# Kernel optimization log

Hardware: AMD Instinct MI355X
Metric: run time of the kernel (lower is better)

The kernel has to match this reference:

```python
import jax, jax.numpy as jnp
import numpy as np

GRID_MIN, GRID_MAX, NUM_GRIDS = -2.0, 2.0, 8
DENOM = (GRID_MAX - GRID_MIN) / (NUM_GRIDS - 1)
DIM, NUM_HEADS = 768, 12
B, N = 8, 1024


def _layer_norm(x, w, b, eps=1e-5):
    mu = jnp.mean(x, axis=-1, keepdims=True)
    var = jnp.mean((x - mu) ** 2, axis=-1, keepdims=True)
    return (x - mu) * jax.lax.rsqrt(var + eps) * w + b


def _fastkan(x, ln_w, ln_b, spline_w, base_w, base_b):
    # x: [..., C]; spline_w: [C*G, O]; base_w: [C, O]
    grid = jnp.linspace(GRID_MIN, GRID_MAX, NUM_GRIDS, dtype=x.dtype)
    h = _layer_norm(x, ln_w, ln_b)
    # RBF basis expansion: [..., C, G]
    basis = jnp.exp(-(((h[..., None] - grid) / DENOM) ** 2))
    basis = basis.reshape(*basis.shape[:-2], -1)  # [..., C*G]
    ret = basis @ spline_w
    ret = ret + jax.nn.silu(x) @ base_w + base_b
    return ret


def setup_inputs() -> dict:
    key = jax.random.key(0)
    ks = jax.random.split(key, 6)
    C = DIM
    return {
        "x": jax.random.normal(ks[0], (B, N, C), jnp.float32),
        "qkv_ln_w": jnp.ones((C,), jnp.float32),
        "qkv_ln_b": jnp.zeros((C,), jnp.float32),
        "qkv_spline_w": jax.random.normal(ks[1], (C * NUM_GRIDS, 3 * C), jnp.float32) * 0.1,
        "qkv_base_w": jax.random.normal(ks[2], (C, 3 * C), jnp.float32) * (1.0 / np.sqrt(C)),
        "qkv_base_b": jnp.zeros((3 * C,), jnp.float32),
        "proj_ln_w": jnp.ones((C,), jnp.float32),
        "proj_ln_b": jnp.zeros((C,), jnp.float32),
        "proj_spline_w": jax.random.normal(ks[3], (C * NUM_GRIDS, C), jnp.float32) * 0.1,
        "proj_base_w": jax.random.normal(ks[4], (C, C), jnp.float32) * (1.0 / np.sqrt(C)),
        "proj_base_b": jnp.zeros((C,), jnp.float32),
    }


def reference(x, qkv_ln_w, qkv_ln_b, qkv_spline_w, qkv_base_w, qkv_base_b,
              proj_ln_w, proj_ln_b, proj_spline_w, proj_base_w, proj_base_b):
    b, n, c = x.shape
    h = NUM_HEADS
    d = c // h
    scale = d ** -0.5
    qkv = _fastkan(x, qkv_ln_w, qkv_ln_b, qkv_spline_w, qkv_base_w, qkv_base_b)
    qkv = qkv.reshape(b, n, 3, h, d).transpose(2, 0, 3, 1, 4)  # [3,B,H,N,D]
    q, k, v = qkv[0], qkv[1], qkv[2]
    attn = jnp.einsum("bhnd,bhmd->bhnm", q, k) * scale
    attn = jax.nn.softmax(attn, axis=-1)
    out = jnp.einsum("bhnm,bhmd->bhnd", attn, v)
    out = out.transpose(0, 2, 1, 3).reshape(b, n, c)
    out = _fastkan(out, proj_ln_w, proj_ln_b, proj_spline_w, proj_base_w, proj_base_b)
    return out
```

## Files before the change

kernel.cpp:

```cpp
#include <hip/hip_runtime.h>
#include <cstdint>
#include <cstddef>

typedef _Float16 h8 __attribute__((ext_vector_type(8)));
typedef float f4 __attribute__((ext_vector_type(4)));
typedef float f16f __attribute__((ext_vector_type(16)));

#define DEV static __device__ __forceinline__

DEV void gld16(const void* g, void* l) {
  __builtin_amdgcn_global_load_lds(
      (const __attribute__((address_space(1))) void*)g,
      (__attribute__((address_space(3))) void*)l, 16, 0, 0);
}

__global__ __launch_bounds__(256)
void kan_prep(const float* __restrict__ X, const float* __restrict__ lnw,
              const float* __restrict__ lnb, _Float16* __restrict__ Acat) {
  const int row = blockIdx.x;
  const int tid = threadIdx.x;
  const float* xr = X + (size_t)row * 768;
  float xv[3];
  xv[0] = xr[tid]; xv[1] = xr[tid + 256]; xv[2] = xr[tid + 512];
  float s = xv[0] + xv[1] + xv[2];
  float q = xv[0] * xv[0] + xv[1] * xv[1] + xv[2] * xv[2];
#pragma unroll
  for (int off = 32; off; off >>= 1) {
    s += __shfl_xor(s, off);
    q += __shfl_xor(q, off);
  }
  __shared__ float rs_[4], rq_[4];
  const int wave = tid >> 6;
  if ((tid & 63) == 0) { rs_[wave] = s; rq_[wave] = q; }
  __syncthreads();
  s = rs_[0] + rs_[1] + rs_[2] + rs_[3];
  q = rq_[0] + rq_[1] + rq_[2] + rq_[3];
  const float mu = s * (1.0f / 768.0f);
  const float var = q * (1.0f / 768.0f) - mu * mu;
  const float rsig = rsqrtf(var + 1e-5f);
  _Float16* out = Acat + (size_t)row * 6912;
#pragma unroll
  for (int i = 0; i < 3; ++i) {
    const int c = tid + i * 256;
    const float x = xv[i];
    const float h = (x - mu) * rsig * lnw[c] + lnb[c];
    union { h8 v; _Float16 u[8]; } bs;
#pragma unroll
    for (int g = 0; g < 8; ++g) {
      const float gv = -2.0f + (4.0f / 7.0f) * (float)g;
      const float t = (h - gv) * 1.75f;
      bs.u[g] = (_Float16)__expf(-t * t);
    }
    *(h8*)(out + c * 8) = bs.v;
    out[6144 + c] = (_Float16)(x / (1.0f + __expf(-x)));
  }
}

__global__ __launch_bounds__(256)
void wt_cast(const float* __restrict__ W, _Float16* __restrict__ Bp,
             int N, int koff, int nkt) {
  __shared__ float t[32][33];
  const int k0 = blockIdx.x * 32, n0 = blockIdx.y * 32;
  const int tx = threadIdx.x & 31, ty = threadIdx.x >> 5;
#pragma unroll
  for (int i = 0; i < 4; ++i)
    t[ty + i * 8][tx] = W[(size_t)(k0 + ty + i * 8) * N + n0 + tx];
  __syncthreads();
  const int f = threadIdx.x;
  if (f < 128) {
    const int nn = f & 31, cc = f >> 5;
    union { h8 v; _Float16 u[8]; } bs;
#pragma unroll
    for (int j = 0; j < 8; ++j) bs.u[j] = (_Float16)t[cc * 8 + j][nn];
    const int kg = koff + k0 + cc * 8;
    const int nt = (n0 + nn) >> 5;
    const size_t addr = ((size_t)nt * nkt + (kg >> 6)) * 2048 +
                        (size_t)((((kg >> 4) & 3) * 64 + nn + 32 * ((kg >> 3) & 1))) * 8;
    *(h8*)(Bp + addr) = bs.v;
  }
}

__global__ __launch_bounds__(256)
void v_transpose(const _Float16* __restrict__ qkv, _Float16* __restrict__ Vt) {
  const int bh = blockIdx.z, hh = bh % 12, b = bh / 12;
  const int kvb = blockIdx.x * 32, db = blockIdx.y * 32;
  __shared__ _Float16 t[32][33];
  const int tx = threadIdx.x & 31, ty = threadIdx.x >> 5;
#pragma unroll
  for (int i = 0; i < 4; ++i) {
    const int kv = kvb + ty + i * 8;
    t[ty + i * 8][tx] = qkv[(size_t)(b * 1024 + kv) * 2304 + 1536 + hh * 64 + db + tx];
  }
  __syncthreads();
#pragma unroll
  for (int i = 0; i < 4; ++i) {
    const int d = db + ty + i * 8;
    Vt[(size_t)(bh * 64 + d) * 1024 + kvb + tx] = t[tx][ty + i * 8];
  }
}

#define LOAD_B(dst)                                       \
  {                                                       \
    _Pragma("unroll") for (int ni = 0; ni < 2; ++ni) {    \
      _Pragma("unroll") for (int ks = 0; ks < 4; ++ks)    \
        dst[ni][ks] = *(const h8*)(bpp[ni] + ks * 512);   \
      bpp[ni] += 2048;                                    \
    }                                                     \
  }
#define LOAD_A(buf)                                       \
  {                                                       \
    _Pragma("unroll") for (int i = 0; i < 4; ++i) {       \
      gld16(ap[i], (buf) + alOff[i]);                     \
      ap[i] += 64;                                        \
    }                                                     \
  }
#define MFMA_STEP(buf, br)                                \
  {                                                       \
    const h8* A8 = (const h8*)(buf);                      \
    _Pragma("unroll") for (int ks = 0; ks < 4; ++ks) {    \
      const int o = (ks * 2 + half) ^ swz;                \
      h8 af0 = A8[(wm + l31) * 8 + o];                    \
      h8 af1 = A8[(wm + 32 + l31) * 8 + o];               \
      acc[0][0] = __builtin_amdgcn_mfma_f32_32x32x16_f16(af0, br[0][ks], acc[0][0], 0, 0, 0); \
      acc[0][1] = __builtin_amdgcn_mfma_f32_32x32x16_f16(af0, br[1][ks], acc[0][1], 0, 0, 0); \
      acc[1][0] = __builtin_amdgcn_mfma_f32_32x32x16_f16(af1, br[0][ks], acc[1][0], 0, 0, 0); \
      acc[1][1] = __builtin_amdgcn_mfma_f32_32x32x16_f16(af1, br[1][ks], acc[1][1], 0, 0, 0); \
    }                                                     \
  }

template <bool F16OUT>
__global__ __launch_bounds__(256, 2)
void gemm_bt(const _Float16* __restrict__ A, const _Float16* __restrict__ Bp,
             const float* __restrict__ bias, void* __restrict__ Cout,
             int N, int ldK, int kLen, size_t sliceStride) {
  __shared__ __align__(16) _Float16 As[2 * 128 * 64];
  _Float16* As0 = As;
  _Float16* As1 = As + 128 * 64;
  const int tid = threadIdx.x;
  const int lane = tid & 63, wave = tid >> 6;
  const int gx = gridDim.x;
  const int lin = blockIdx.y * gx + blockIdx.x;
  const int xcd = lin & 7, pos = lin >> 3;
  const int bandH = gridDim.y >> 3;
  const int bm = (xcd * bandH + pos / gx) * 128;
  const int bn = (pos % gx) * 128;
  const int slice = blockIdx.z;
  const int kOff = slice * kLen;
  const int rsub = lane >> 3;
  const int l7 = lane & 7;
  const int l31 = lane & 31, half = lane >> 5;
  const int wm = (wave >> 1) * 64, wn = (wave & 1) * 64;
  const _Float16* ap[4];
  int alOff[4];
#pragma unroll
  for (int i = 0; i < 4; ++i) {
    const int ch = wave * 4 + i;
    const int ksw = (l7 ^ rsub ^ ((ch & 3) << 1)) * 8;
    ap[i] = A + (size_t)(bm + ch * 8 + rsub) * ldK + kOff + ksw;
    alOff[i] = ch * 512;
  }
  const size_t nktTot = (size_t)(ldK >> 6);
  const int kt0 = kOff >> 6;
  const _Float16* bpp[2];
#pragma unroll
  for (int ni = 0; ni < 2; ++ni)
    bpp[ni] = Bp + ((size_t)((bn >> 5) + (wn >> 5) + ni) * nktTot + kt0) * 2048 + lane * 8;

  f16f acc[2][2] = {};
  const int swz = l7 ^ ((rsub & 3) << 1);
  const int nkt = kLen >> 6;
  h8 bregA[2][4], bregB[2][4];
  LOAD_B(bregA);
  LOAD_A(As0);
  for (int kt = 0; kt < nkt; kt += 2) {
    __syncthreads();
    if (kt + 1 < nkt) { LOAD_B(bregB); LOAD_A(As1); }
    MFMA_STEP(As0, bregA);
    __syncthreads();
    if (kt + 2 < nkt) { LOAD_B(bregA); LOAD_A(As0); }
    MFMA_STEP(As1, bregB);
  }
#pragma unroll
  for (int ni = 0; ni < 2; ++ni) {
    const int col = bn + wn + ni * 32 + l31;
    const float bv = F16OUT ? bias[col] : 0.0f;
#pragma unroll
    for (int mi = 0; mi < 2; ++mi) {
      const int rb = bm + wm + mi * 32 + 4 * half;
#pragma unroll
      for (int reg = 0; reg < 16; ++reg) {
        const int r = rb + (reg & 3) + 8 * (reg >> 2);
        const float v = acc[mi][ni][reg] + bv;
        if (F16OUT)
          ((_Float16*)Cout)[(size_t)r * N + col] = (_Float16)v;
        else
          ((float*)Cout + slice * sliceStride)[(size_t)r * N + col] = v;
      }
    }
  }
}

__global__ __launch_bounds__(256)
void ksum2(const float* __restrict__ P, const float* __restrict__ bias,
           float* __restrict__ out) {
  const size_t off = ((size_t)blockIdx.x * 256 + threadIdx.x) * 4;
  const int col = (int)(off % 768);
  f4 a = *(const f4*)(P + off);
  f4 b = *(const f4*)(P + (size_t)8192 * 768 + off);
  f4 c = *(const f4*)(bias + col);
  *(f4*)(out + off) = a + b + c;
}

__global__ __launch_bounds__(256)
void attn(const _Float16* __restrict__ qkv, const _Float16* __restrict__ Vt,
          float* __restrict__ ctx) {
  __shared__ __align__(16) _Float16 Qs[128 * 64];
  __shared__ __align__(16) _Float16 Ks[64 * 64];
  __shared__ __align__(16) _Float16 Vs[64 * 64];
  __shared__ __align__(16) _Float16 Ps[4 * 32 * 72];
  const int tid = threadIdx.x;
  const int lane = tid & 63, wave = tid >> 6;
  const int bh = blockIdx.y, hh = bh % 12, b = bh / 12;
  const int qt = blockIdx.x;
  const int rsub = lane >> 3;
  const int ksw = ((lane & 7) ^ rsub) * 8;
#pragma unroll
  for (int i = 0; i < 4; ++i) {
    const int ch = wave * 4 + i;
    const int row = ch * 8 + rsub;
    gld16(qkv + (size_t)(b * 1024 + qt * 128 + row) * 2304 + hh * 64 + ksw, Qs + ch * 512);
  }
  const int l16 = lane & 15, quad = lane >> 4, r7 = l16 & 7;
  f4 acc_o[2][4] = {};
  float m_old[2][4], l_sum[2][4];
#pragma unroll
  for (int mi = 0; mi < 2; ++mi)
#pragma unroll
    for (int j = 0; j < 4; ++j) { m_old[mi][j] = -1e30f; l_sum[mi][j] = 0.0f; }

  _Float16* Pw = Ps + wave * (32 * 72);

  for (int kv0 = 0; kv0 < 1024; kv0 += 64) {
#pragma unroll
    for (int i = 0; i < 2; ++i) {
      const int ch = wave * 2 + i;
      const int row = ch * 8 + rsub;
      gld16(qkv + (size_t)(b * 1024 + kv0 + row) * 2304 + 768 + hh * 64 + ksw, Ks + ch * 512);
      gld16(Vt + (size_t)(bh * 64 + row) * 1024 + kv0 + ksw, Vs + ch * 512);
    }
    __syncthreads();
    const h8* Q8 = (const h8*)Qs;
    const h8* K8 = (const h8*)Ks;
    const h8* V8 = (const h8*)Vs;
    f4 s[2][4] = {};
#pragma unroll
    for (int ks = 0; ks < 2; ++ks) {
      const int kq = (ks * 4 + quad) ^ r7;
      h8 qf[2], kf[4];
#pragma unroll
      for (int mi = 0; mi < 2; ++mi) qf[mi] = Q8[(wave * 32 + mi * 16 + l16) * 8 + kq];
#pragma unroll
      for (int ni = 0; ni < 4; ++ni) kf[ni] = K8[(ni * 16 + l16) * 8 + kq];
#pragma unroll
      for (int mi = 0; mi < 2; ++mi)
#pragma unroll
        for (int ni = 0; ni < 4; ++ni)
          s[mi][ni] = __builtin_amdgcn_mfma_f32_16x16x32_f16(qf[mi], kf[ni], s[mi][ni], 0, 0, 0);
    }
#pragma unroll
    for (int mi = 0; mi < 2; ++mi)
#pragma unroll
      for (int ni = 0; ni < 4; ++ni) s[mi][ni] *= 0.125f;
#pragma unroll
    for (int mi = 0; mi < 2; ++mi) {
#pragma unroll
      for (int j = 0; j < 4; ++j) {
        float vm = fmaxf(fmaxf(s[mi][0][j], s[mi][1][j]), fmaxf(s[mi][2][j], s[mi][3][j]));
#pragma unroll
        for (int off = 1; off < 16; off <<= 1) vm = fmaxf(vm, __shfl_xor(vm, off));
        const float mn = fmaxf(m_old[mi][j], vm);
        const float alpha = __expf(m_old[mi][j] - mn);
        float rs = 0.0f;
#pragma unroll
        for (int ni = 0; ni < 4; ++ni) {
          const float p = __expf(s[mi][ni][j] - mn);
          s[mi][ni][j] = p;
          rs += p;
        }
#pragma unroll
        for (int off = 1; off < 16; off <<= 1) rs += __shfl_xor(rs, off);
        l_sum[mi][j] = l_sum[mi][j] * alpha + rs;
        m_old[mi][j] = mn;
#pragma unroll
        for (int ni = 0; ni < 4; ++ni) acc_o[mi][ni][j] *= alpha;
      }
    }
#pragma unroll
    for (int mi = 0; mi < 2; ++mi)
#pragma unroll
      for (int ni = 0; ni < 4; ++ni)
#pragma unroll
        for (int j = 0; j < 4; ++j)
          Pw[(mi * 16 + quad * 4 + j) * 72 + ni * 16 + l16] = (_Float16)s[mi][ni][j];
#pragma unroll
    for (int ks = 0; ks < 2; ++ks) {
      const int kq = ks * 4 + quad;
      h8 pf[2], vf[4];
#pragma unroll
      for (int mi = 0; mi < 2; ++mi) pf[mi] = *(const h8*)(Pw + (mi * 16 + l16) * 72 + kq * 8);
#pragma unroll
      for (int ni = 0; ni < 4; ++ni) vf[ni] = V8[(ni * 16 + l16) * 8 + (kq ^ r7)];
#pragma unroll
      for (int mi = 0; mi < 2; ++mi)
#pragma unroll
        for (int ni = 0; ni < 4; ++ni)
          acc_o[mi][ni] = __builtin_amdgcn_mfma_f32_16x16x32_f16(pf[mi], vf[ni], acc_o[mi][ni], 0, 0, 0);
    }
    __syncthreads();
  }
#pragma unroll
  for (int mi = 0; mi < 2; ++mi) {
#pragma unroll
    for (int j = 0; j < 4; ++j) {
      const float inv = 1.0f / l_sum[mi][j];
      const int tok = b * 1024 + qt * 128 + wave * 32 + mi * 16 + quad * 4 + j;
      float* cr = ctx + (size_t)tok * 768 + hh * 64;
#pragma unroll
      for (int ni = 0; ni < 4; ++ni) cr[ni * 16 + l16] = acc_o[mi][ni][j] * inv;
    }
  }
}

extern "C" void kernel_launch(void* const* d_in, const int* in_sizes, int n_in,
                              void* d_out, int out_size, void* d_ws, size_t ws_size,
                              hipStream_t stream) {
  (void)in_sizes; (void)n_in; (void)out_size; (void)ws_size;
  const float* x    = (const float*)d_in[0];
  const float* qlnw = (const float*)d_in[1];
  const float* qlnb = (const float*)d_in[2];
  const float* qsw  = (const float*)d_in[3];
  const float* qbw  = (const float*)d_in[4];
  const float* qbb  = (const float*)d_in[5];
  const float* plnw = (const float*)d_in[6];
  const float* plnb = (const float*)d_in[7];
  const float* psw  = (const float*)d_in[8];
  const float* pbw  = (const float*)d_in[9];
  const float* pbb  = (const float*)d_in[10];
  float* out = (float*)d_out;

  _Float16* WtQ  = (_Float16*)d_ws;
  _Float16* WtP  = WtQ + (size_t)2304 * 6912;
  _Float16* Acat = WtP + (size_t)768 * 6912;
  _Float16* QKV  = Acat + (size_t)8192 * 6912;
  _Float16* Vt   = QKV + (size_t)8192 * 2304;
  float* CTX = (float*)(Vt + (size_t)96 * 64 * 1024);
  float* Pp = (float*)QKV;

  dim3 blk(256);
  wt_cast<<<dim3(192, 72), blk, 0, stream>>>(qsw, WtQ, 2304, 0, 108);
  wt_cast<<<dim3(24, 72),  blk, 0, stream>>>(qbw, WtQ, 2304, 6144, 108);
  wt_cast<<<dim3(192, 24), blk, 0, stream>>>(psw, WtP, 768, 0, 108);
  wt_cast<<<dim3(24, 24),  blk, 0, stream>>>(pbw, WtP, 768, 6144, 108);
  kan_prep<<<8192, blk, 0, stream>>>(x, qlnw, qlnb, Acat);
  gemm_bt<true><<<dim3(2304 / 128, 8192 / 128, 1), blk, 0, stream>>>(
      Acat, WtQ, qbb, QKV, 2304, 6912, 6912, 0);
  v_transpose<<<dim3(32, 2, 96), blk, 0, stream>>>(QKV, Vt);
  attn<<<dim3(8, 96), blk, 0, stream>>>(QKV, Vt, CTX);
  kan_prep<<<8192, blk, 0, stream>>>(CTX, plnw, plnb, Acat);
  gemm_bt<false><<<dim3(768 / 128, 8192 / 128, 2), blk, 0, stream>>>(
      Acat, WtP, nullptr, Pp, 768, 6912, 3456, (size_t)8192 * 768);
  ksum2<<<8192 * 768 / 4 / 256, blk, 0, stream>>>(Pp, pbb, out);
}
```

Before: 712.1 us.

## Use 8-wave 256x128 tile GEMM with priority-boosted MFMA for QKV projection

Adds a new gemm8 kernel with 512 threads per block and a 256x128 output tile for the QKV KAN GEMM. B fragments go straight into registers through double-buffered register sets, and A is double-buffered in LDS. Synchronisation uses explicit waitcnt/barrier and sched_barrier, and s_setprio is raised around the MFMA sections. The larger tile increases reuse of the B fragments and halves the grid along M. In exchange it uses more LDS and registers per block, which may lower occupancy, and the hand-tuned wait counts carry a correctness risk.

```diff
diff --git a/kernel.cpp b/kernel.cpp
--- a/kernel.cpp
+++ b/kernel.cpp
@@ -127,6 +127,91 @@
       acc[1][1] = __builtin_amdgcn_mfma_f32_32x32x16_f16(af1, br[1][ks], acc[1][1], 0, 0, 0); \
     }                                                     \
   }
+#define SB() __builtin_amdgcn_sched_barrier(0)
+#define WAITBAR()                                                        \
+  {                                                                      \
+    asm volatile("s_waitcnt vmcnt(8) lgkmcnt(0)" ::: "memory");          \
+    __builtin_amdgcn_s_barrier();                                        \
+    asm volatile("" ::: "memory");                                       \
+  }
+#define COMPUTE(buf, br)                                  \
+  {                                                       \
+    __builtin_amdgcn_s_setprio(1);                        \
+    MFMA_STEP(buf, br);                                   \
+    __builtin_amdgcn_s_setprio(0);                        \
+  }
+
+__global__ __launch_bounds__(512, 2)
+void gemm8(const _Float16* __restrict__ A, const _Float16* __restrict__ Bp,
+           const float* __restrict__ bias, _Float16* __restrict__ Cout,
+           int N, int ldK) {
+  __shared__ __align__(16) _Float16 As[2 * 256 * 64];
+  _Float16* As0 = As;
+  _Float16* As1 = As + 256 * 64;
+  const int tid = threadIdx.x;
+  const int lane = tid & 63, wave = tid >> 6;
+  const int gx = gridDim.x;
+  const int lin = blockIdx.y * gx + blockIdx.x;
+  const int xcd = lin & 7, pos = lin >> 3;
+  const int bandH = gridDim.y >> 3;
+  const int bm = (xcd * bandH + pos / gx) * 256;
+  const int bn = (pos % gx) * 128;
+  const int rsub = lane >> 3;
+  const int l7 = lane & 7;
+  const int l31 = lane & 31, half = lane >> 5;
+  const int wm = (wave >> 1) * 64, wn = (wave & 1) * 64;
+  const _Float16* ap[4];
+  int alOff[4];
+#pragma unroll
+  for (int i = 0; i < 4; ++i) {
+    const int ch = wave * 4 + i;
+    const int ksw = (l7 ^ rsub ^ ((ch & 3) << 1)) * 8;
+    ap[i] = A + (size_t)(bm + ch * 8 + rsub) * ldK + ksw;
+    alOff[i] = ch * 512;
+  }
+  const size_t nktTot = (size_t)(ldK >> 6);
+  const _Float16* bpp[2];
+#pragma unroll
+  for (int ni = 0; ni < 2; ++ni)
+    bpp[ni] = Bp + (size_t)((bn >> 5) + (wn >> 5) + ni) * nktTot * 2048 + lane * 8;
+
+  f16f acc[2][2] = {};
+  const int swz = l7 ^ ((rsub & 3) << 1);
+  const int nkt = ldK >> 6;
+  h8 bregA[2][4], bregB[2][4];
+  LOAD_A(As0); SB();
+  LOAD_B(bregA); SB();
+  WAITBAR();
+  for (int kt = 0; kt < nkt - 2; kt += 2) {
+    LOAD_A(As1); SB();
+    LOAD_B(bregB); SB();
+    COMPUTE(As0, bregA);
+    WAITBAR();
+    LOAD_A(As0); SB();
+    LOAD_B(bregA); SB();
+    COMPUTE(As1, bregB);
+    WAITBAR();
+  }
+  LOAD_A(As1); SB();
+  LOAD_B(bregB); SB();
+  COMPUTE(As0, bregA);
+  WAITBAR();
+  COMPUTE(As1, bregB);
+#pragma unroll
+  for (int ni = 0; ni < 2; ++ni) {
+    const int col = bn + wn + ni * 32 + l31;
+    const float bv = bias[col];
+#pragma unroll
+    for (int mi = 0; mi < 2; ++mi) {
+      const int rb = bm + wm + mi * 32 + 4 * half;
+#pragma unroll
+      for (int reg = 0; reg < 16; ++reg) {
+        const int r = rb + (reg & 3) + 8 * (reg >> 2);
+        Cout[(size_t)r * N + col] = (_Float16)(acc[mi][ni][reg] + bv);
+      }
+    }
+  }
+}
 
 template <bool F16OUT>
 __global__ __launch_bounds__(256, 2)
@@ -362,8 +447,8 @@
   wt_cast<<<dim3(192, 24), blk, 0, stream>>>(psw, WtP, 768, 0, 108);
   wt_cast<<<dim3(24, 24),  blk, 0, stream>>>(pbw, WtP, 768, 6144, 108);
   kan_prep<<<8192, blk, 0, stream>>>(x, qlnw, qlnb, Acat);
-  gemm_bt<true><<<dim3(2304 / 128, 8192 / 128, 1), blk, 0, stream>>>(
-      Acat, WtQ, qbb, QKV, 2304, 6912, 6912, 0);
+  gemm8<<<dim3(2304 / 128, 8192 / 256), dim3(512), 0, stream>>>(
+      Acat, WtQ, qbb, QKV, 2304, 6912);
   v_transpose<<<dim3(32, 2, 96), blk, 0, stream>>>(QKV, Vt);
   attn<<<dim3(8, 96), blk, 0, stream>>>(QKV, Vt, CTX);
   kan_prep<<<8192, blk, 0, stream>>>(CTX, plnw, plnb, Acat);
```

New measurement: 789.6 us. 10.9% more time.

## Triple-buffer A tiles in GEMM with explicit vmcnt waits and sched barriers

Applied to the files above, without the earlier changes.

Replaces the double-buffered LDS pipeline in the GEMM kernel with a three-stage ring buffer. A tiles are prefetched two steps ahead, and each step waits on a partial vmcnt count instead of a full __syncthreads, with sched_barrier pinning the instruction order. The aim is to keep more global loads in flight and hide their latency behind the MFMAs. It uses 50% more LDS per block, which can lower occupancy, and the hard-coded epilogue assumes nkt is large enough and follows a specific stage pattern.

```diff
diff --git a/kernel.cpp b/kernel.cpp
--- a/kernel.cpp
+++ b/kernel.cpp
@@ -127,15 +127,21 @@
       acc[1][1] = __builtin_amdgcn_mfma_f32_32x32x16_f16(af1, br[1][ks], acc[1][1], 0, 0, 0); \
     }                                                     \
   }
+#define SB() __builtin_amdgcn_sched_barrier(0)
+#define WB(n)                                                          \
+  {                                                                    \
+    asm volatile("s_waitcnt vmcnt(" #n ") lgkmcnt(0)" ::: "memory");   \
+    __builtin_amdgcn_s_barrier();                                      \
+    SB();                                                              \
+  }
 
 template <bool F16OUT>
 __global__ __launch_bounds__(256, 2)
 void gemm_bt(const _Float16* __restrict__ A, const _Float16* __restrict__ Bp,
              const float* __restrict__ bias, void* __restrict__ Cout,
              int N, int ldK, int kLen, size_t sliceStride) {
-  __shared__ __align__(16) _Float16 As[2 * 128 * 64];
-  _Float16* As0 = As;
-  _Float16* As1 = As + 128 * 64;
+  __shared__ __align__(16) _Float16 As[3 * 128 * 64];
+  _Float16* const bufs[3] = {As, As + 8192, As + 16384};
   const int tid = threadIdx.x;
   const int lane = tid & 63, wave = tid >> 6;
   const int gx = gridDim.x;
@@ -170,16 +176,23 @@
   const int swz = l7 ^ ((rsub & 3) << 1);
   const int nkt = kLen >> 6;
   h8 bregA[2][4], bregB[2][4];
-  LOAD_B(bregA);
-  LOAD_A(As0);
-  for (int kt = 0; kt < nkt; kt += 2) {
-    __syncthreads();
-    if (kt + 1 < nkt) { LOAD_B(bregB); LOAD_A(As1); }
-    MFMA_STEP(As0, bregA);
-    __syncthreads();
-    if (kt + 2 < nkt) { LOAD_B(bregA); LOAD_A(As0); }
-    MFMA_STEP(As1, bregB);
-  }
+  LOAD_A(bufs[0]); SB();
+  LOAD_A(bufs[1]); SB();
+  LOAD_B(bregA); SB();
+  for (int kt = 0; kt < nkt - 6; kt += 6) {
+    WB(12); LOAD_B(bregB); SB(); LOAD_A(bufs[2]); SB(); MFMA_STEP(bufs[0], bregA);
+    WB(12); LOAD_B(bregA); SB(); LOAD_A(bufs[0]); SB(); MFMA_STEP(bufs[1], bregB);
+    WB(12); LOAD_B(bregB); SB(); LOAD_A(bufs[1]); SB(); MFMA_STEP(bufs[2], bregA);
+    WB(12); LOAD_B(bregA); SB(); LOAD_A(bufs[2]); SB(); MFMA_STEP(bufs[0], bregB);
+    WB(12); LOAD_B(bregB); SB(); LOAD_A(bufs[0]); SB(); MFMA_STEP(bufs[1], bregA);
+    WB(12); LOAD_B(bregA); SB(); LOAD_A(bufs[1]); SB(); MFMA_STEP(bufs[2], bregB);
+  }
+  WB(12); LOAD_B(bregB); SB(); LOAD_A(bufs[2]); SB(); MFMA_STEP(bufs[0], bregA);
+  WB(12); LOAD_B(bregA); SB(); LOAD_A(bufs[0]); SB(); MFMA_STEP(bufs[1], bregB);
+  WB(12); LOAD_B(bregB); SB(); LOAD_A(bufs[1]); SB(); MFMA_STEP(bufs[2], bregA);
+  WB(12); LOAD_B(bregA); SB(); LOAD_A(bufs[2]); SB(); MFMA_STEP(bufs[0], bregB);
+  WB(12); LOAD_B(bregB); SB();                        MFMA_STEP(bufs[1], bregA);
+  WB(8);                                              MFMA_STEP(bufs[2], bregB);
 #pragma unroll
   for (int ni = 0; ni < 2; ++ni) {
     const int col = bn + wn + ni * 32 + l31;
```

Result: slower. 741.4 us (+4.1%).

## Triple-buffer GEMM A tiles and double-buffer attention K/V with Q in registers

Applied to the files above, without the earlier changes.

The GEMM moves from a two-stage to a three-stage LDS ring for A tiles, using explicit vmcnt-based waits plus barriers so that two tile loads stay in flight during MFMA work. The attention kernel keeps Q fragments in registers instead of LDS, double-buffers K/V so the next tile is prefetched while the current one is computed, folds the 1/8 scale into the exp argument, and raises wave priority around MFMA sections. The aim is to hide global-load latency and cut barrier stalls. The cost is more LDS in the GEMM, which may lower occupancy. The hand-written waitcnt counts are fragile: they assume a fixed number of outstanding loads per stage.

```diff
diff --git a/kernel.cpp b/kernel.cpp
--- a/kernel.cpp
+++ b/kernel.cpp
@@ -127,15 +127,21 @@
       acc[1][1] = __builtin_amdgcn_mfma_f32_32x32x16_f16(af1, br[1][ks], acc[1][1], 0, 0, 0); \
     }                                                     \
   }
+#define WB(n)                                                          \
+  {                                                                    \
+    asm volatile("s_waitcnt vmcnt(" #n ") lgkmcnt(0)" ::: "memory");   \
+    __builtin_amdgcn_s_barrier();                                      \
+  }
 
 template <bool F16OUT>
 __global__ __launch_bounds__(256, 2)
 void gemm_bt(const _Float16* __restrict__ A, const _Float16* __restrict__ Bp,
              const float* __restrict__ bias, void* __restrict__ Cout,
              int N, int ldK, int kLen, size_t sliceStride) {
-  __shared__ __align__(16) _Float16 As[2 * 128 * 64];
-  _Float16* As0 = As;
-  _Float16* As1 = As + 128 * 64;
+  __shared__ __align__(16) _Float16 As[3 * 128 * 64];
+  _Float16* const b0 = As;
+  _Float16* const b1 = As + 8192;
+  _Float16* const b2 = As + 16384;
   const int tid = threadIdx.x;
   const int lane = tid & 63, wave = tid >> 6;
   const int gx = gridDim.x;
@@ -170,16 +176,23 @@
   const int swz = l7 ^ ((rsub & 3) << 1);
   const int nkt = kLen >> 6;
   h8 bregA[2][4], bregB[2][4];
+  LOAD_A(b0);
+  LOAD_A(b1);
   LOAD_B(bregA);
-  LOAD_A(As0);
-  for (int kt = 0; kt < nkt; kt += 2) {
-    __syncthreads();
-    if (kt + 1 < nkt) { LOAD_B(bregB); LOAD_A(As1); }
-    MFMA_STEP(As0, bregA);
-    __syncthreads();
-    if (kt + 2 < nkt) { LOAD_B(bregA); LOAD_A(As0); }
-    MFMA_STEP(As1, bregB);
-  }
+  for (int kt = 0; kt < nkt - 6; kt += 6) {
+    WB(12); LOAD_B(bregB); LOAD_A(b2); MFMA_STEP(b0, bregA);
+    WB(12); LOAD_B(bregA); LOAD_A(b0); MFMA_STEP(b1, bregB);
+    WB(12); LOAD_B(bregB); LOAD_A(b1); MFMA_STEP(b2, bregA);
+    WB(12); LOAD_B(bregA); LOAD_A(b2); MFMA_STEP(b0, bregB);
+    WB(12); LOAD_B(bregB); LOAD_A(b0); MFMA_STEP(b1, bregA);
+    WB(12); LOAD_B(bregA); LOAD_A(b1); MFMA_STEP(b2, bregB);
+  }
+  WB(12); LOAD_B(bregB); LOAD_A(b2); MFMA_STEP(b0, bregA);
+  WB(12); LOAD_B(bregA); LOAD_A(b0); MFMA_STEP(b1, bregB);
+  WB(12); LOAD_B(bregB); LOAD_A(b1); MFMA_STEP(b2, bregA);
+  WB(12); LOAD_B(bregA); LOAD_A(b2); MFMA_STEP(b0, bregB);
+  WB(12); LOAD_B(bregB);             MFMA_STEP(b1, bregA);
+  WB(8);                             MFMA_STEP(b2, bregB);
 #pragma unroll
   for (int ni = 0; ni < 2; ++ni) {
     const int col = bn + wn + ni * 32 + l31;
@@ -211,12 +224,16 @@
   *(f4*)(out + off) = a + b + c;
 }
 
+#define WBA()                                                          \
+  {                                                                    \
+    asm volatile("s_waitcnt vmcnt(0) lgkmcnt(0)" ::: "memory");        \
+    __builtin_amdgcn_s_barrier();                                      \
+  }
 __global__ __launch_bounds__(256)
 void attn(const _Float16* __restrict__ qkv, const _Float16* __restrict__ Vt,
           float* __restrict__ ctx) {
-  __shared__ __align__(16) _Float16 Qs[128 * 64];
-  __shared__ __align__(16) _Float16 Ks[64 * 64];
-  __shared__ __align__(16) _Float16 Vs[64 * 64];
+  __shared__ __align__(16) _Float16 Ks[2][64 * 64];
+  __shared__ __align__(16) _Float16 Vs[2][64 * 64];
   __shared__ __align__(16) _Float16 Ps[4 * 32 * 72];
   const int tid = threadIdx.x;
   const int lane = tid & 63, wave = tid >> 6;
@@ -224,13 +241,22 @@
   const int qt = blockIdx.x;
   const int rsub = lane >> 3;
   const int ksw = ((lane & 7) ^ rsub) * 8;
-#pragma unroll
-  for (int i = 0; i < 4; ++i) {
-    const int ch = wave * 4 + i;
+  const int l16 = lane & 15, quad = lane >> 4, r7 = l16 & 7;
+  h8 qreg[2][2];
+#pragma unroll
+  for (int mi = 0; mi < 2; ++mi)
+#pragma unroll
+    for (int ks = 0; ks < 2; ++ks) {
+      const size_t row = (size_t)(b * 1024 + qt * 128 + wave * 32 + mi * 16 + l16);
+      qreg[mi][ks] = *(const h8*)(qkv + row * 2304 + hh * 64 + (ks * 4 + quad) * 8);
+    }
+#pragma unroll
+  for (int i = 0; i < 2; ++i) {
+    const int ch = wave * 2 + i;
     const int row = ch * 8 + rsub;
-    gld16(qkv + (size_t)(b * 1024 + qt * 128 + row) * 2304 + hh * 64 + ksw, Qs + ch * 512);
-  }
-  const int l16 = lane & 15, quad = lane >> 4, r7 = l16 & 7;
+    gld16(qkv + (size_t)(b * 1024 + row) * 2304 + 768 + hh * 64 + ksw, Ks[0] + ch * 512);
+    gld16(Vt + (size_t)(bh * 64 + row) * 1024 + ksw, Vs[0] + ch * 512);
+  }
   f4 acc_o[2][4] = {};
   float m_old[2][4], l_sum[2][4];
 #pragma unroll
@@ -240,37 +266,37 @@
 
   _Float16* Pw = Ps + wave * (32 * 72);
 
-  for (int kv0 = 0; kv0 < 1024; kv0 += 64) {
-#pragma unroll
-    for (int i = 0; i < 2; ++i) {
-      const int ch = wave * 2 + i;
-      const int row = ch * 8 + rsub;
-      gld16(qkv + (size_t)(b * 1024 + kv0 + row) * 2304 + 768 + hh * 64 + ksw, Ks + ch * 512);
-      gld16(Vt + (size_t)(bh * 64 + row) * 1024 + kv0 + ksw, Vs + ch * 512);
-    }
-    __syncthreads();
-    const h8* Q8 = (const h8*)Qs;
-    const h8* K8 = (const h8*)Ks;
-    const h8* V8 = (const h8*)Vs;
+  for (int it = 0; it < 16; ++it) {
+    WBA();
+    if (it < 15) {
+      const int kvn = (it + 1) * 64;
+#pragma unroll
+      for (int i = 0; i < 2; ++i) {
+        const int ch = wave * 2 + i;
+        const int row = ch * 8 + rsub;
+        gld16(qkv + (size_t)(b * 1024 + kvn + row) * 2304 + 768 + hh * 64 + ksw,
+              Ks[(it + 1) & 1] + ch * 512);
+        gld16(Vt + (size_t)(bh * 64 + row) * 1024 + kvn + ksw,
+              Vs[(it + 1) & 1] + ch * 512);
+      }
+    }
+    const h8* K8 = (const h8*)Ks[it & 1];
+    const h8* V8 = (const h8*)Vs[it & 1];
     f4 s[2][4] = {};
+    __builtin_amdgcn_s_setprio(1);
 #pragma unroll
     for (int ks = 0; ks < 2; ++ks) {
       const int kq = (ks * 4 + quad) ^ r7;
-      h8 qf[2], kf[4];
-#pragma unroll
-      for (int mi = 0; mi < 2; ++mi) qf[mi] = Q8[(wave * 32 + mi * 16 + l16) * 8 + kq];
+      h8 kf[4];
 #pragma unroll
       for (int ni = 0; ni < 4; ++ni) kf[ni] = K8[(ni * 16 + l16) * 8 + kq];
 #pragma unroll
       for (int mi = 0; mi < 2; ++mi)
 #pragma unroll
         for (int ni = 0; ni < 4; ++ni)
-          s[mi][ni] = __builtin_amdgcn_mfma_f32_16x16x32_f16(qf[mi], kf[ni], s[mi][ni], 0, 0, 0);
-    }
-#pragma unroll
-    for (int mi = 0; mi < 2; ++mi)
-#pragma unroll
-      for (int ni = 0; ni < 4; ++ni) s[mi][ni] *= 0.125f;
+          s[mi][ni] = __builtin_amdgcn_mfma_f32_16x16x32_f16(qreg[mi][ks], kf[ni], s[mi][ni], 0, 0, 0);
+    }
+    __builtin_amdgcn_s_setprio(0);
 #pragma unroll
     for (int mi = 0; mi < 2; ++mi) {
 #pragma unroll
@@ -279,11 +305,11 @@
 #pragma unroll
         for (int off = 1; off < 16; off <<= 1) vm = fmaxf(vm, __shfl_xor(vm, off));
         const float mn = fmaxf(m_old[mi][j], vm);
-        const float alpha = __expf(m_old[mi][j] - mn);
+        const float alpha = __expf((m_old[mi][j] - mn) * 0.125f);
         float rs = 0.0f;
 #pragma unroll
         for (int ni = 0; ni < 4; ++ni) {
-          const float p = __expf(s[mi][ni][j] - mn);
+          const float p = __expf((s[mi][ni][j] - mn) * 0.125f);
           s[mi][ni][j] = p;
           rs += p;
         }
@@ -302,6 +328,7 @@
 #pragma unroll
         for (int j = 0; j < 4; ++j)
           Pw[(mi * 16 + quad * 4 + j) * 72 + ni * 16 + l16] = (_Float16)s[mi][ni][j];
+    __builtin_amdgcn_s_setprio(1);
 #pragma unroll
     for (int ks = 0; ks < 2; ++ks) {
       const int kq = ks * 4 + quad;
@@ -316,7 +343,7 @@
         for (int ni = 0; ni < 4; ++ni)
           acc_o[mi][ni] = __builtin_amdgcn_mfma_f32_16x16x32_f16(pf[mi], vf[ni], acc_o[mi][ni], 0, 0, 0);
     }
-    __syncthreads();
+    __builtin_amdgcn_s_setprio(0);
   }
 #pragma unroll
   for (int mi = 0; mi < 2; ++mi) {
```

Measured after the change: 760.2 us. 1.07x slower.
